# Optimization experiments

Measured on AMD Instinct MI355X. Metric: run time of the kernel, lower is better.

The kernel has to match this reference:

```python
import jax, jax.numpy as jnp
import numpy as np

D = 256      # x_size
Y = 256      # y_size (c0 / SRU hidden)
H = D // 4   # attention hidden = 64
A = 8        # n_actions


def setup_inputs() -> dict:
    key = jax.random.key(0)
    ks = jax.random.split(key, 10)
    B, L = 32, 2048
    stdv = 1.0 / np.sqrt(H)
    x = jax.random.normal(ks[0], (B, L, D), dtype=jnp.float32)
    c0 = jax.random.normal(ks[1], (B, Y), dtype=jnp.float32)
    x_mask = jnp.zeros((B, L), dtype=bool)
    actions = jax.random.randint(ks[2], (B,), 0, A)
    w1 = jax.random.uniform(ks[3], (A, D, H), minval=-stdv, maxval=stdv, dtype=jnp.float32)
    b1 = jnp.zeros((A, H), dtype=jnp.float32)
    w2 = jax.random.uniform(ks[4], (A, Y, H), minval=-stdv, maxval=stdv, dtype=jnp.float32)
    b2 = jnp.zeros((A, H), dtype=jnp.float32)
    v = jax.random.uniform(ks[5], (A, H), minval=-stdv, maxval=stdv, dtype=jnp.float32)
    # SRU cell weights: input D -> hidden Y, k=3 blocks (x_tilde, f-gate, r-gate)
    w_sru = jax.random.uniform(ks[6], (D, 3 * Y), minval=-stdv, maxval=stdv, dtype=jnp.float32)
    b_sru = jnp.zeros((2 * Y,), dtype=jnp.float32)
    return {"x": x, "x_mask": x_mask, "c0": c0, "actions": actions,
            "w1": w1, "b1": b1, "w2": w2, "b2": b2, "v": v,
            "w_sru": w_sru, "b_sru": b_sru}


def _attention(x, y, x_mask, actions, w1, b1, w2, b2, v):
    # Gather per-batch action params (original does one-hot matmul + expand; same math)
    w1a = w1[actions]            # [B, D, H]
    w2a = w2[actions]            # [B, Y, H]
    b1a = b1[actions]            # [B, H]
    b2a = b2[actions]            # [B, H]
    va = v[actions]              # [B, H]
    x_t = jnp.einsum('bld,bdh->blh', x, w1a) + b1a[:, None, :]
    y_t = jnp.einsum('bd,bdh->bh', y, w2a) + b2a
    inpt = jnp.tanh(x_t + y_t[:, None, :])          # [B, L, H]
    scores = jnp.einsum('blh,bh->bl', inpt, va)      # [B, L]
    return jnp.where(x_mask, -jnp.inf, scores)


def _sru_cell_c(attn_pool, c0, w_sru, b_sru):
    # single-step SRU: c = f * c0 + (1 - f) * x_tilde ; forward()[1] returns c
    u = attn_pool @ w_sru                             # [B, 3Y]
    x_tilde = u[:, :Y]
    f = jax.nn.sigmoid(u[:, Y:2 * Y] + b_sru[:Y])
    return f * c0 + (1.0 - f) * x_tilde


def reference(x, x_mask, c0, actions, w1, b1, w2, b2, v, w_sru, b_sru):
    s_logits = _attention(x, c0, x_mask, actions, w1, b1, w2, b2, v)
    s_probs = jax.nn.softmax(s_logits, axis=-1)
    attn_pool = jnp.einsum('bld,bl->bd', x, s_probs)  # [B, D]
    state = _sru_cell_c(attn_pool, c0, w_sru, b_sru)  # [B, Y]
    e_logits = _attention(x, state, x_mask, actions, w1, b1, w2, b2, v)
    # eval mode: softmax
    return jax.nn.softmax(s_logits, axis=-1), jax.nn.softmax(e_logits, axis=-1)
```

## Files before the change

kernel.cpp:

```cpp
#include <hip/hip_runtime.h>
#include <math.h>

#define B 32
#define L 2048
#define D 256
#define H 64

__global__ __launch_bounds__(256) void k1_setup(
    const float* __restrict__ c0, const int* __restrict__ actions,
    const float* __restrict__ w2, const float* __restrict__ b2,
    float* __restrict__ y_ts, float* __restrict__ pool) {
  int b = blockIdx.x;
  int t = threadIdx.x;
  __shared__ float c0s[D];
  c0s[t] = c0[b * D + t];
  pool[b * D + t] = 0.0f;
  __syncthreads();
  if (t < H) {
    int a = actions[b];
    const float* w = w2 + (size_t)a * D * H;
    float s = b2[a * H + t];
    #pragma unroll 8
    for (int d = 0; d < D; ++d) s += c0s[d] * w[d * H + t];
    y_ts[b * H + t] = s;
  }
}

#define LB 128
#define DK 32
#define XS_STRIDE 36

__global__ __launch_bounds__(256) void k2_xt_scores(
    const float* __restrict__ x, const int* __restrict__ actions,
    const float* __restrict__ w1, const float* __restrict__ b1,
    const float* __restrict__ v, const float* __restrict__ y_ts,
    float* __restrict__ xt, float* __restrict__ s_logits) {
  int b  = blockIdx.y;
  int l0 = blockIdx.x * LB;
  int t  = threadIdx.x;
  int th = t & 15;
  int tr = t >> 4;
  int a  = actions[b];
  const float* w1a = w1 + (size_t)a * D * H;
  const float* xb  = x + ((size_t)b * L + l0) * D;

  __shared__ float xs[LB * XS_STRIDE];
  __shared__ float wsd[DK * H];

  float acc[8][4];
  #pragma unroll
  for (int i = 0; i < 8; ++i)
    #pragma unroll
    for (int j = 0; j < 4; ++j) acc[i][j] = 0.0f;

  for (int d0 = 0; d0 < D; d0 += DK) {
    __syncthreads();
    {
      const float4* g = (const float4*)(w1a + (size_t)d0 * H);
      float4* s = (float4*)wsd;
      s[t] = g[t];
      s[t + 256] = g[t + 256];
    }
    #pragma unroll
    for (int k = 0; k < 4; ++k) {
      int f4  = t + k * 256;
      int row = f4 >> 3;
      int col = f4 & 7;
      float4 val = *(const float4*)(xb + (size_t)row * D + d0 + col * 4);
      *(float4*)&xs[row * XS_STRIDE + col * 4] = val;
    }
    __syncthreads();
    #pragma unroll
    for (int dd = 0; dd < DK; dd += 4) {
      float xr[8][4];
      #pragma unroll
      for (int i = 0; i < 8; ++i)
        *(float4*)xr[i] = *(const float4*)&xs[(tr * 8 + i) * XS_STRIDE + dd];
      float wr[4][4];
      #pragma unroll
      for (int k = 0; k < 4; ++k)
        *(float4*)wr[k] = *(const float4*)&wsd[(dd + k) * H + th * 4];
      #pragma unroll
      for (int i = 0; i < 8; ++i)
        #pragma unroll
        for (int k = 0; k < 4; ++k)
          #pragma unroll
          for (int j = 0; j < 4; ++j)
            acc[i][j] += xr[i][k] * wr[k][j];
    }
  }

  float bb[4], vv[4], yy[4];
  #pragma unroll
  for (int j = 0; j < 4; ++j) {
    int h = th * 4 + j;
    bb[j] = b1[a * H + h];
    vv[j] = v[a * H + h];
    yy[j] = y_ts[b * H + h];
  }
  #pragma unroll
  for (int i = 0; i < 8; ++i) {
    int l = l0 + tr * 8 + i;
    float4 o;
    o.x = acc[i][0] + bb[0];
    o.y = acc[i][1] + bb[1];
    o.z = acc[i][2] + bb[2];
    o.w = acc[i][3] + bb[3];
    *(float4*)(xt + ((size_t)b * L + l) * H + th * 4) = o;
    float p = vv[0] * tanhf(o.x + yy[0]) + vv[1] * tanhf(o.y + yy[1])
            + vv[2] * tanhf(o.z + yy[2]) + vv[3] * tanhf(o.w + yy[3]);
    #pragma unroll
    for (int off = 1; off < 16; off <<= 1) p += __shfl_xor(p, off);
    if (th == 0) s_logits[b * L + l] = p;
  }
}

__global__ __launch_bounds__(256) void k_softmax(
    const float* __restrict__ logits, float* __restrict__ out) {
  int b = blockIdx.x;
  int t = threadIdx.x;
  __shared__ float red[4];
  float vals[8];
  float m = -1e30f;
  #pragma unroll
  for (int i = 0; i < 8; ++i) {
    vals[i] = logits[b * L + t + i * 256];
    m = fmaxf(m, vals[i]);
  }
  #pragma unroll
  for (int off = 1; off < 64; off <<= 1) m = fmaxf(m, __shfl_xor(m, off));
  int w = t >> 6;
  if ((t & 63) == 0) red[w] = m;
  __syncthreads();
  m = fmaxf(fmaxf(red[0], red[1]), fmaxf(red[2], red[3]));
  float s = 0.0f;
  #pragma unroll
  for (int i = 0; i < 8; ++i) {
    vals[i] = expf(vals[i] - m);
    s += vals[i];
  }
  #pragma unroll
  for (int off = 1; off < 64; off <<= 1) s += __shfl_xor(s, off);
  __syncthreads();
  if ((t & 63) == 0) red[w] = s;
  __syncthreads();
  s = red[0] + red[1] + red[2] + red[3];
  float inv = 1.0f / s;
  #pragma unroll
  for (int i = 0; i < 8; ++i) out[b * L + t + i * 256] = vals[i] * inv;
}

__global__ __launch_bounds__(256) void k4_pool(
    const float* __restrict__ x, const float* __restrict__ probs,
    float* __restrict__ pool) {
  int b  = blockIdx.y;
  int l0 = blockIdx.x * 128;
  int d  = threadIdx.x;
  const float* xb = x + ((size_t)b * L + l0) * D;
  const float* pb = probs + b * L + l0;
  float a0 = 0, a1 = 0, a2 = 0, a3 = 0;
  for (int i = 0; i < 128; i += 4) {
    a0 += pb[i]     * xb[(size_t)(i)     * D + d];
    a1 += pb[i + 1] * xb[(size_t)(i + 1) * D + d];
    a2 += pb[i + 2] * xb[(size_t)(i + 2) * D + d];
    a3 += pb[i + 3] * xb[(size_t)(i + 3) * D + d];
  }
  atomicAdd(&pool[b * D + d], (a0 + a1) + (a2 + a3));
}

__global__ __launch_bounds__(256) void k5_sru(
    const float* __restrict__ pool, const float* __restrict__ c0,
    const float* __restrict__ w_sru, const float* __restrict__ b_sru,
    const int* __restrict__ actions, const float* __restrict__ w2,
    const float* __restrict__ b2, float* __restrict__ y_te) {
  int b = blockIdx.x;
  int t = threadIdx.x;
  __shared__ float pl[D];
  __shared__ float st[D];
  pl[t] = pool[b * D + t];
  __syncthreads();
  float u0 = 0.0f, u1 = 0.0f;
  #pragma unroll 4
  for (int d = 0; d < D; ++d) {
    float pd = pl[d];
    u0 += pd * w_sru[(size_t)d * 768 + t];
    u1 += pd * w_sru[(size_t)d * 768 + 256 + t];
  }
  float f = 1.0f / (1.0f + expf(-(u1 + b_sru[t])));
  st[t] = f * c0[b * D + t] + (1.0f - f) * u0;
  __syncthreads();
  if (t < H) {
    int a = actions[b];
    const float* w = w2 + (size_t)a * D * H;
    float s = b2[a * H + t];
    #pragma unroll 8
    for (int d = 0; d < D; ++d) s += st[d] * w[d * H + t];
    y_te[b * H + t] = s;
  }
}

__global__ __launch_bounds__(256) void k6_escores(
    const float* __restrict__ xt, const float* __restrict__ y_te,
    const float* __restrict__ v, const int* __restrict__ actions,
    float* __restrict__ e_logits) {
  int b    = blockIdx.y;
  int t    = threadIdx.x;
  int lane = t & 63;
  int wv   = t >> 6;
  int l0   = blockIdx.x * 32;
  int a    = actions[b];
  float yv = y_te[b * H + lane];
  float vv = v[a * H + lane];
  #pragma unroll
  for (int i = 0; i < 8; ++i) {
    int l = l0 + wv * 8 + i;
    float xv = xt[((size_t)b * L + l) * H + lane];
    float p = vv * tanhf(xv + yv);
    #pragma unroll
    for (int off = 1; off < 64; off <<= 1) p += __shfl_xor(p, off);
    if (lane == 0) e_logits[b * L + l] = p;
  }
}

extern "C" void kernel_launch(void* const* d_in, const int* in_sizes, int n_in,
                              void* d_out, int out_size, void* d_ws, size_t ws_size,
                              hipStream_t stream) {
  const float* x       = (const float*)d_in[0];
  const float* c0      = (const float*)d_in[2];
  const int*   actions = (const int*)d_in[3];
  const float* w1      = (const float*)d_in[4];
  const float* b1      = (const float*)d_in[5];
  const float* w2      = (const float*)d_in[6];
  const float* b2      = (const float*)d_in[7];
  const float* v       = (const float*)d_in[8];
  const float* w_sru   = (const float*)d_in[9];
  const float* b_sru   = (const float*)d_in[10];
  float* out = (float*)d_out;

  float* ws       = (float*)d_ws;
  float* xt       = ws;
  float* s_logits = xt + (size_t)B * L * H;
  float* e_logits = s_logits + B * L;
  float* y_ts     = e_logits + B * L;
  float* y_te     = y_ts + B * H;
  float* pool     = y_te + B * H;

  k1_setup<<<B, 256, 0, stream>>>(c0, actions, w2, b2, y_ts, pool);
  k2_xt_scores<<<dim3(L / LB, B), 256, 0, stream>>>(x, actions, w1, b1, v, y_ts,
                                                    xt, s_logits);
  k_softmax<<<B, 256, 0, stream>>>(s_logits, out);
  k4_pool<<<dim3(16, B), 256, 0, stream>>>(x, out, pool);
  k5_sru<<<B, 256, 0, stream>>>(pool, c0, w_sru, b_sru, actions, w2, b2, y_te);
  k6_escores<<<dim3(L / 32, B), 256, 0, stream>>>(xt, y_te, v, actions, e_logits);
  k_softmax<<<B, 256, 0, stream>>>(e_logits, out + B * L);
}
```

Before: 199.1 us.

## Fuse setup, pool and SRU kernels; enlarge GEMM tiles; vectorize e-score pass

Folds the y_ts computation into the x·W1 kernel, so every block recomputes the c0·W2 projection and the separate setup launch goes away. Doubles the K tile and gives each of 128 threads an 8x8 accumulator. The pool kernel now loads x as float4 and runs the SRU step and the second projection in the last block per batch, chosen with an atomic counter. The pool zeroing moves into the first softmax kernel. The e-score kernel reads xt as float4 with 16-lane reductions. This removes two launches and some memory traffic, at the cost of redundant per-block work, atomic/threadfence synchronization and higher register pressure.

```diff
diff --git a/kernel.cpp b/kernel.cpp
--- a/kernel.cpp
+++ b/kernel.cpp
@@ -6,66 +6,66 @@
 #define D 256
 #define H 64
 
-__global__ __launch_bounds__(256) void k1_setup(
-    const float* __restrict__ c0, const int* __restrict__ actions,
-    const float* __restrict__ w2, const float* __restrict__ b2,
-    float* __restrict__ y_ts, float* __restrict__ pool) {
-  int b = blockIdx.x;
-  int t = threadIdx.x;
-  __shared__ float c0s[D];
-  c0s[t] = c0[b * D + t];
-  pool[b * D + t] = 0.0f;
-  __syncthreads();
-  if (t < H) {
-    int a = actions[b];
-    const float* w = w2 + (size_t)a * D * H;
-    float s = b2[a * H + t];
-    #pragma unroll 8
-    for (int d = 0; d < D; ++d) s += c0s[d] * w[d * H + t];
-    y_ts[b * H + t] = s;
-  }
-}
-
 #define LB 128
-#define DK 32
-#define XS_STRIDE 36
-
-__global__ __launch_bounds__(256) void k2_xt_scores(
+#define DK 64
+#define XS_STRIDE 68
+
+__global__ __launch_bounds__(128) void k2_xt_scores(
     const float* __restrict__ x, const int* __restrict__ actions,
     const float* __restrict__ w1, const float* __restrict__ b1,
-    const float* __restrict__ v, const float* __restrict__ y_ts,
+    const float* __restrict__ w2, const float* __restrict__ b2,
+    const float* __restrict__ c0, const float* __restrict__ v,
     float* __restrict__ xt, float* __restrict__ s_logits) {
   int b  = blockIdx.y;
   int l0 = blockIdx.x * LB;
   int t  = threadIdx.x;
-  int th = t & 15;
-  int tr = t >> 4;
+  int th = t & 7;
+  int tr = t >> 3;
   int a  = actions[b];
   const float* w1a = w1 + (size_t)a * D * H;
   const float* xb  = x + ((size_t)b * L + l0) * D;
 
   __shared__ float xs[LB * XS_STRIDE];
   __shared__ float wsd[DK * H];
-
-  float acc[8][4];
+  __shared__ float c0s[D];
+  __shared__ float ysp[2 * H];
+  __shared__ float ys[H];
+
+  c0s[t] = c0[b * D + t];
+  c0s[t + 128] = c0[b * D + t + 128];
+  __syncthreads();
+  {
+    int h = t & 63;
+    int part = t >> 6;
+    const float* w = w2 + (size_t)a * D * H;
+    float s = 0.0f;
+    #pragma unroll 8
+    for (int d = part * 128; d < part * 128 + 128; ++d)
+      s += c0s[d] * w[d * H + h];
+    ysp[part * H + h] = s;
+  }
+  __syncthreads();
+  if (t < H) ys[t] = ysp[t] + ysp[H + t] + b2[a * H + t];
+
+  float acc[8][8];
   #pragma unroll
   for (int i = 0; i < 8; ++i)
     #pragma unroll
-    for (int j = 0; j < 4; ++j) acc[i][j] = 0.0f;
+    for (int j = 0; j < 8; ++j) acc[i][j] = 0.0f;
 
   for (int d0 = 0; d0 < D; d0 += DK) {
     __syncthreads();
     {
       const float4* g = (const float4*)(w1a + (size_t)d0 * H);
       float4* s = (float4*)wsd;
-      s[t] = g[t];
-      s[t + 256] = g[t + 256];
-    }
-    #pragma unroll
-    for (int k = 0; k < 4; ++k) {
-      int f4  = t + k * 256;
-      int row = f4 >> 3;
-      int col = f4 & 7;
+      #pragma unroll
+      for (int k = 0; k < 8; ++k) s[t + k * 128] = g[t + k * 128];
+    }
+    #pragma unroll
+    for (int k = 0; k < 16; ++k) {
+      int f4  = t + k * 128;
+      int row = f4 >> 4;
+      int col = f4 & 15;
       float4 val = *(const float4*)(xb + (size_t)row * D + d0 + col * 4);
       *(float4*)&xs[row * XS_STRIDE + col * 4] = val;
     }
@@ -75,50 +75,59 @@
       float xr[8][4];
       #pragma unroll
       for (int i = 0; i < 8; ++i)
-        *(float4*)xr[i] = *(const float4*)&xs[(tr * 8 + i) * XS_STRIDE + dd];
-      float wr[4][4];
-      #pragma unroll
-      for (int k = 0; k < 4; ++k)
-        *(float4*)wr[k] = *(const float4*)&wsd[(dd + k) * H + th * 4];
+        *(float4*)xr[i] = *(const float4*)&xs[(tr + 16 * i) * XS_STRIDE + dd];
+      float wr[4][8];
+      #pragma unroll
+      for (int k = 0; k < 4; ++k) {
+        *(float4*)&wr[k][0] = *(const float4*)&wsd[(dd + k) * H + th * 8];
+        *(float4*)&wr[k][4] = *(const float4*)&wsd[(dd + k) * H + th * 8 + 4];
+      }
       #pragma unroll
       for (int i = 0; i < 8; ++i)
         #pragma unroll
         for (int k = 0; k < 4; ++k)
           #pragma unroll
-          for (int j = 0; j < 4; ++j)
+          for (int j = 0; j < 8; ++j)
             acc[i][j] += xr[i][k] * wr[k][j];
     }
   }
 
-  float bb[4], vv[4], yy[4];
-  #pragma unroll
-  for (int j = 0; j < 4; ++j) {
-    int h = th * 4 + j;
+  float bb[8], vv[8], yy[8];
+  #pragma unroll
+  for (int j = 0; j < 8; ++j) {
+    int h = th * 8 + j;
     bb[j] = b1[a * H + h];
     vv[j] = v[a * H + h];
-    yy[j] = y_ts[b * H + h];
+    yy[j] = ys[h];
   }
   #pragma unroll
   for (int i = 0; i < 8; ++i) {
-    int l = l0 + tr * 8 + i;
-    float4 o;
-    o.x = acc[i][0] + bb[0];
-    o.y = acc[i][1] + bb[1];
-    o.z = acc[i][2] + bb[2];
-    o.w = acc[i][3] + bb[3];
-    *(float4*)(xt + ((size_t)b * L + l) * H + th * 4) = o;
-    float p = vv[0] * tanhf(o.x + yy[0]) + vv[1] * tanhf(o.y + yy[1])
-            + vv[2] * tanhf(o.z + yy[2]) + vv[3] * tanhf(o.w + yy[3]);
-    #pragma unroll
-    for (int off = 1; off < 16; off <<= 1) p += __shfl_xor(p, off);
+    int l = l0 + tr + 16 * i;
+    float o[8];
+    float p = 0.0f;
+    #pragma unroll
+    for (int j = 0; j < 8; ++j) {
+      o[j] = acc[i][j] + bb[j];
+      p += vv[j] * tanhf(o[j] + yy[j]);
+    }
+    float* xrow = xt + ((size_t)b * L + l) * H + th * 8;
+    *(float4*)xrow = *(float4*)&o[0];
+    *(float4*)(xrow + 4) = *(float4*)&o[4];
+    #pragma unroll
+    for (int off = 1; off < 8; off <<= 1) p += __shfl_xor(p, off);
     if (th == 0) s_logits[b * L + l] = p;
   }
 }
 
 __global__ __launch_bounds__(256) void k_softmax(
-    const float* __restrict__ logits, float* __restrict__ out) {
+    const float* __restrict__ logits, float* __restrict__ out,
+    float* __restrict__ pool, int* __restrict__ cnt) {
   int b = blockIdx.x;
   int t = threadIdx.x;
+  if (pool) {
+    pool[b * D + t] = 0.0f;
+    if (t == 0) cnt[b] = 0;
+  }
   __shared__ float red[4];
   float vals[8];
   float m = -1e30f;
@@ -150,53 +159,78 @@
   for (int i = 0; i < 8; ++i) out[b * L + t + i * 256] = vals[i] * inv;
 }
 
-__global__ __launch_bounds__(256) void k4_pool(
+__global__ __launch_bounds__(256) void k4_pool_sru(
     const float* __restrict__ x, const float* __restrict__ probs,
-    float* __restrict__ pool) {
-  int b  = blockIdx.y;
-  int l0 = blockIdx.x * 128;
-  int d  = threadIdx.x;
-  const float* xb = x + ((size_t)b * L + l0) * D;
-  const float* pb = probs + b * L + l0;
-  float a0 = 0, a1 = 0, a2 = 0, a3 = 0;
-  for (int i = 0; i < 128; i += 4) {
-    a0 += pb[i]     * xb[(size_t)(i)     * D + d];
-    a1 += pb[i + 1] * xb[(size_t)(i + 1) * D + d];
-    a2 += pb[i + 2] * xb[(size_t)(i + 2) * D + d];
-    a3 += pb[i + 3] * xb[(size_t)(i + 3) * D + d];
-  }
-  atomicAdd(&pool[b * D + d], (a0 + a1) + (a2 + a3));
-}
-
-__global__ __launch_bounds__(256) void k5_sru(
-    const float* __restrict__ pool, const float* __restrict__ c0,
-    const float* __restrict__ w_sru, const float* __restrict__ b_sru,
-    const int* __restrict__ actions, const float* __restrict__ w2,
-    const float* __restrict__ b2, float* __restrict__ y_te) {
-  int b = blockIdx.x;
-  int t = threadIdx.x;
-  __shared__ float pl[D];
+    const float* __restrict__ c0, const float* __restrict__ w_sru,
+    const float* __restrict__ b_sru, const int* __restrict__ actions,
+    const float* __restrict__ w2, const float* __restrict__ b2,
+    float* __restrict__ pool, int* __restrict__ cnt,
+    float* __restrict__ y_te) {
+  int b    = blockIdx.y;
+  int l0   = blockIdx.x * 128;
+  int t    = threadIdx.x;
+  int w    = t >> 6;
+  int lane = t & 63;
+  __shared__ float ps[128];
+  if (t < 128) ps[t] = probs[b * L + l0 + t];
+  __syncthreads();
+  const float4* xb4 = (const float4*)(x + ((size_t)b * L + l0) * D);
+  float4 acc = make_float4(0.f, 0.f, 0.f, 0.f);
+  #pragma unroll 4
+  for (int ii = 0; ii < 32; ++ii) {
+    int i = w + ii * 4;
+    float4 xv = xb4[(size_t)i * 64 + lane];
+    float p = ps[i];
+    acc.x += p * xv.x; acc.y += p * xv.y;
+    acc.z += p * xv.z; acc.w += p * xv.w;
+  }
+  float* pb = pool + b * D + lane * 4;
+  atomicAdd(pb + 0, acc.x);
+  atomicAdd(pb + 1, acc.y);
+  atomicAdd(pb + 2, acc.z);
+  atomicAdd(pb + 3, acc.w);
+
+  __shared__ int is_last;
+  __threadfence();
+  __syncthreads();
+  if (t == 0) is_last = (atomicAdd(&cnt[b], 1) == 15);
+  __syncthreads();
+  if (!is_last) return;
+  __threadfence();
   __shared__ float st[D];
-  pl[t] = pool[b * D + t];
-  __syncthreads();
+  __shared__ float yp[4 * H];
   float u0 = 0.0f, u1 = 0.0f;
+  {
+    float pv = atomicAdd(&pool[b * D + t], 0.0f);
+    st[t] = pv;
+  }
+  __syncthreads();
   #pragma unroll 4
   for (int d = 0; d < D; ++d) {
-    float pd = pl[d];
+    float pd = st[d];
     u0 += pd * w_sru[(size_t)d * 768 + t];
     u1 += pd * w_sru[(size_t)d * 768 + 256 + t];
   }
   float f = 1.0f / (1.0f + expf(-(u1 + b_sru[t])));
-  st[t] = f * c0[b * D + t] + (1.0f - f) * u0;
-  __syncthreads();
-  if (t < H) {
-    int a = actions[b];
-    const float* w = w2 + (size_t)a * D * H;
-    float s = b2[a * H + t];
+  float sv = f * c0[b * D + t] + (1.0f - f) * u0;
+  __syncthreads();
+  st[t] = sv;
+  __syncthreads();
+  int a = actions[b];
+  {
+    int h = t & 63;
+    int part = t >> 6;
+    const float* wv = w2 + (size_t)a * D * H;
+    float s = 0.0f;
     #pragma unroll 8
-    for (int d = 0; d < D; ++d) s += st[d] * w[d * H + t];
-    y_te[b * H + t] = s;
-  }
+    for (int d = part * 64; d < part * 64 + 64; ++d)
+      s += st[d] * wv[d * H + h];
+    yp[part * H + h] = s;
+  }
+  __syncthreads();
+  if (t < H)
+    y_te[b * H + t] = yp[t] + yp[H + t] + yp[2 * H + t] + yp[3 * H + t]
+                    + b2[a * H + t];
 }
 
 __global__ __launch_bounds__(256) void k6_escores(
@@ -205,20 +239,24 @@
     float* __restrict__ e_logits) {
   int b    = blockIdx.y;
   int t    = threadIdx.x;
+  int w    = t >> 6;
   int lane = t & 63;
-  int wv   = t >> 6;
-  int l0   = blockIdx.x * 32;
+  int th   = lane & 15;
+  int rg   = lane >> 4;
+  int base = blockIdx.x * 64 + w * 16;
   int a    = actions[b];
-  float yv = y_te[b * H + lane];
-  float vv = v[a * H + lane];
-  #pragma unroll
-  for (int i = 0; i < 8; ++i) {
-    int l = l0 + wv * 8 + i;
-    float xv = xt[((size_t)b * L + l) * H + lane];
-    float p = vv * tanhf(xv + yv);
-    #pragma unroll
-    for (int off = 1; off < 64; off <<= 1) p += __shfl_xor(p, off);
-    if (lane == 0) e_logits[b * L + l] = p;
+  float4 yy = *(const float4*)(y_te + b * H + th * 4);
+  float4 vv = *(const float4*)(v + a * H + th * 4);
+  const float4* xt4 = (const float4*)(xt + (size_t)b * L * H);
+  #pragma unroll
+  for (int i = 0; i < 4; ++i) {
+    int r = base + rg + 4 * i;
+    float4 xv = xt4[(size_t)r * 16 + th];
+    float p = vv.x * tanhf(xv.x + yy.x) + vv.y * tanhf(xv.y + yy.y)
+            + vv.z * tanhf(xv.z + yy.z) + vv.w * tanhf(xv.w + yy.w);
+    #pragma unroll
+    for (int off = 1; off < 16; off <<= 1) p += __shfl_xor(p, off);
+    if (th == 0) e_logits[b * L + r] = p;
   }
 }
 
@@ -241,16 +279,15 @@
   float* xt       = ws;
   float* s_logits = xt + (size_t)B * L * H;
   float* e_logits = s_logits + B * L;
-  float* y_ts     = e_logits + B * L;
-  float* y_te     = y_ts + B * H;
+  float* y_te     = e_logits + B * L;
   float* pool     = y_te + B * H;
-
-  k1_setup<<<B, 256, 0, stream>>>(c0, actions, w2, b2, y_ts, pool);
-  k2_xt_scores<<<dim3(L / LB, B), 256, 0, stream>>>(x, actions, w1, b1, v, y_ts,
-                                                    xt, s_logits);
-  k_softmax<<<B, 256, 0, stream>>>(s_logits, out);
-  k4_pool<<<dim3(16, B), 256, 0, stream>>>(x, out, pool);
-  k5_sru<<<B, 256, 0, stream>>>(pool, c0, w_sru, b_sru, actions, w2, b2, y_te);
-  k6_escores<<<dim3(L / 32, B), 256, 0, stream>>>(xt, y_te, v, actions, e_logits);
-  k_softmax<<<B, 256, 0, stream>>>(e_logits, out + B * L);
-}
+  int*   cnt      = (int*)(pool + B * D);
+
+  k2_xt_scores<<<dim3(L / LB, B), 128, 0, stream>>>(
+      x, actions, w1, b1, w2, b2, c0, v, xt, s_logits);
+  k_softmax<<<B, 256, 0, stream>>>(s_logits, out, pool, cnt);
+  k4_pool_sru<<<dim3(16, B), 256, 0, stream>>>(
+      x, out, c0, w_sru, b_sru, actions, w2, b2, pool, cnt, y_te);
+  k6_escores<<<dim3(L / 64, B), 256, 0, stream>>>(xt, y_te, v, actions, e_logits);
+  k_softmax<<<B, 256, 0, stream>>>(e_logits, out + B * L, nullptr, nullptr);
+}
```

New measurement: 236.1 us. 1.19x slower.
